# Performance work log

Measured on AMD Instinct MI355X. Metric: run time of the kernel, lower is better.

Reference implementation:

```python
import jax, jax.numpy as jnp
import numpy as np

B, D, F, E, G = 2048, 1024, 4096, 16, 2
EPS = 1e-9
LN_EPS = 1e-5


def setup_inputs() -> dict:
    key = jax.random.key(0)
    ks = jax.random.split(key, 10)
    s_in = 1.0 / np.sqrt(D)
    s_out = 1.0 / np.sqrt(F)
    return {
        "cycle_curve_data": jax.random.normal(ks[0], (B, D), jnp.float32),
        "logits": jax.random.normal(ks[1], (B, E), jnp.float32),
        "moe_masks": jax.random.randint(ks[2], (B, E), 0, 2, jnp.int32),
        "ew_in": jax.random.uniform(ks[3], (E, D, F), jnp.float32, -s_in, s_in),
        "ew_out": jax.random.uniform(ks[4], (E, F, D), jnp.float32, -s_out, s_out),
        "eb_out": jax.random.uniform(ks[5], (E, D), jnp.float32, -s_out, s_out),
        "gw_in": jax.random.uniform(ks[6], (G, D, F), jnp.float32, -s_in, s_in),
        "gw_out": jax.random.uniform(ks[7], (G, F, D), jnp.float32, -s_out, s_out),
        "gb_out": jax.random.uniform(ks[8], (G, D), jnp.float32, -s_out, s_out),
        "ln_gamma": jnp.ones((D,), jnp.float32),
        "ln_beta": jnp.zeros((D,), jnp.float32),
    }


def _moe_forward(x, logits, moe_masks, ew_in, ew_out, eb_out, gw_in, gw_out, gb_out, ln_gamma, ln_beta):
    b = x.shape[0]
    mask = (moe_masks == 1).astype(logits.dtype)          # [B,E]
    raw = jax.nn.softmax(logits, axis=1)                   # [B,E]
    gates = raw * mask
    gates = gates / (jnp.sum(gates, axis=1, keepdims=True) + EPS)
    # Per-expert MLPBlockGELU over all tokens; gate=0 zeroes out non-dispatched
    # tokens exactly as MOEDispatcher.combine does.
    h = jax.nn.gelu(jnp.einsum('bd,edf->ebf', x, ew_in), approximate=False)  # [E,B,F]
    eout = jnp.einsum('ebf,efd->ebd', h, ew_out) + eb_out[:, None, :]        # [E,B,D]
    moe_out = jnp.einsum('be,ebd->bd', gates, eout).astype(jnp.bfloat16)     # combine + bf16 cast
    # general experts (dense, added to routed output; bf16+f32 promotes to f32)
    gh = jax.nn.gelu(jnp.einsum('bd,gdf->gbf', x, gw_in), approximate=False)
    gout = jnp.einsum('gbf,gfd->gbd', gh, gw_out) + gb_out[:, None, :]       # [G,B,D]
    final = jnp.sum(gout, axis=0) + moe_out                                  # f32
    # residual + LayerNorm
    y = final + x
    mu = jnp.mean(y, axis=-1, keepdims=True)
    var = jnp.mean(jnp.square(y - mu), axis=-1, keepdims=True)
    final_out = (y - mu) * jax.lax.rsqrt(var + LN_EPS) * ln_gamma + ln_beta
    # training losses
    expert_logits = jnp.mean(raw, axis=0)                                    # [E]
    expert_sample_count = jnp.sum((gates != 0).astype(raw.dtype), axis=0) / b
    aug_loss = jnp.mean(expert_logits * expert_sample_count)
    s = jnp.sum(raw * mask) / b
    guide_loss = (1.0 - s) * (1.0 - s)
    return final_out, aug_loss, guide_loss


def reference(cycle_curve_data, logits, moe_masks, ew_in, ew_out, eb_out, gw_in, gw_out, gb_out, ln_gamma, ln_beta):
    return _moe_forward(cycle_curve_data, logits, moe_masks, ew_in, ew_out, eb_out,
                        gw_in, gw_out, gb_out, ln_gamma, ln_beta)
```

## Files before the change

kernel.cpp:

```cpp
#include <hip/hip_runtime.h>
#include <hip/hip_bf16.h>

#define B_TOK 2048
#define DDIM 1024
#define FDIM 4096
#define NE 16
#define NG 2
#define BD ((long)B_TOK * DDIM)

typedef unsigned short u16;
typedef __attribute__((ext_vector_type(8))) short bf16x8;
typedef __attribute__((ext_vector_type(4))) float f32x4;

__device__ inline u16 f2bf(float x) {
  union { float f; unsigned u; } v; v.f = x;
  return (u16)((v.u + 0x7fffu + ((v.u >> 16) & 1u)) >> 16);
}
__device__ inline float bfround(float x) {
  union { float f; unsigned u; } v; v.f = x;
  v.u = ((v.u + 0x7fffu + ((v.u >> 16) & 1u)) >> 16) << 16;
  return v.f;
}
__device__ inline float fast_erf(float x) {
  float ax = fabsf(x);
  float t = __builtin_amdgcn_rcpf(1.0f + 0.3275911f * ax);
  float poly = t * (0.254829592f + t * (-0.284496736f + t * (1.421413741f +
               t * (-1.453152027f + t * 1.061405429f))));
  float r = 1.0f - poly * __expf(-ax * ax);
  return copysignf(r, x);
}
__device__ inline float gelu_exact(float x) {
  return 0.5f * x * (1.0f + fast_erf(x * 0.70710678118654752440f));
}
__device__ inline void gload16(const void* g, void* l) {
  __builtin_amdgcn_global_load_lds((const __attribute__((address_space(1))) void*)g,
                                   (__attribute__((address_space(3))) void*)l, 16, 0, 0);
}
__device__ inline float waveSum(float v) {
  v += __shfl_down(v, 32); v += __shfl_down(v, 16); v += __shfl_down(v, 8);
  v += __shfl_down(v, 4);  v += __shfl_down(v, 2);  v += __shfl_down(v, 1);
  return v;
}

__global__ __launch_bounds__(256) void gating_kernel(
    const float* __restrict__ logits, const int* __restrict__ masks,
    float* __restrict__ gates, float* __restrict__ loss)
{
  const int b = blockIdx.x * 256 + threadIdx.x;
  const int lane = threadIdx.x & 63;
  const float* lr = logits + (long)b * NE;
  const int*   mr = masks  + (long)b * NE;
  float raw[NE]; int mk[NE];
  float mx = -1e30f;
#pragma unroll
  for (int e = 0; e < NE; ++e) { raw[e] = lr[e]; mx = fmaxf(mx, raw[e]); }
  float s = 0.f;
#pragma unroll
  for (int e = 0; e < NE; ++e) { raw[e] = expf(raw[e] - mx); s += raw[e]; }
  float inv = 1.0f / s;
#pragma unroll
  for (int e = 0; e < NE; ++e) raw[e] *= inv;
  float gs = 0.f;
#pragma unroll
  for (int e = 0; e < NE; ++e) { mk[e] = (mr[e] == 1); gs += mk[e] ? raw[e] : 0.f; }
  float ginv = 1.0f / (gs + 1e-9f);
  float* gr = gates + (long)b * NE;
#pragma unroll
  for (int e = 0; e < NE; ++e) gr[e] = (mk[e] ? raw[e] : 0.f) * ginv;
#pragma unroll
  for (int e = 0; e < NE; ++e) {
    float cs = waveSum(raw[e]);
    float cc = waveSum(mk[e] ? 1.f : 0.f);
    if (lane == 0) { atomicAdd(&loss[e], cs); atomicAdd(&loss[NE + e], cc); }
  }
  float t = waveSum(gs);
  if (lane == 0) atomicAdd(&loss[32], t);
}

__global__ void finalize_loss(const float* __restrict__ loss, float* __restrict__ out2) {
  if (threadIdx.x == 0) {
    float aug = 0.f;
    for (int e = 0; e < NE; ++e)
      aug += (loss[e] / (float)B_TOK) * (loss[NE + e] / (float)B_TOK);
    aug *= (1.0f / NE);
    float s = loss[32] / (float)B_TOK;
    out2[0] = aug;
    out2[1] = (1.f - s) * (1.f - s);
  }
}

__global__ __launch_bounds__(256) void compact_kernel(
    const int* __restrict__ masks, int* __restrict__ tok,
    int* __restrict__ pos, int* __restrict__ cnts)
{
  const int e = blockIdx.x, tid = threadIdx.x;
  const int lane = tid & 63, wave = tid >> 6;
  __shared__ int wcnt[4];
  __shared__ int runbase;
  if (tid == 0) runbase = 0;
  __syncthreads();
  for (int b0 = 0; b0 < B_TOK; b0 += 256) {
    int b = b0 + tid;
    int m = (masks[(long)b * NE + e] == 1);
    unsigned long long bal = __ballot(m);
    int pre = __popcll(bal & ((1ull << lane) - 1ull));
    if (lane == 0) wcnt[wave] = __popcll(bal);
    __syncthreads();
    int base = runbase;
    for (int w = 0; w < wave; ++w) base += wcnt[w];
    if (m) {
      int p = base + pre;
      tok[(e << 11) + p] = b;
      pos[(long)b * NE + e] = p;
    } else {
      pos[(long)b * NE + e] = -1;
    }
    __syncthreads();
    if (tid == 0) runbase += wcnt[0] + wcnt[1] + wcnt[2] + wcnt[3];
    __syncthreads();
  }
  const int cnt = runbase;
  const int cnt_pad = (cnt + 255) & ~255;
  for (int i = cnt + tid; i < cnt_pad; i += 256)
    tok[(e << 11) + i] = 0;
  if (tid == 0) { cnts[e] = cnt; cnts[NE + e] = cnt_pad; }
}

__global__ __launch_bounds__(256) void cvt_x_kernel(const float* __restrict__ x, u16* __restrict__ xb) {
  long i = ((long)blockIdx.x * 256 + threadIdx.x) * 4;
  float4 v = *(const float4*)&x[i];
  ushort4 o; o.x = f2bf(v.x); o.y = f2bf(v.y); o.z = f2bf(v.z); o.w = f2bf(v.w);
  *(ushort4*)&xb[i] = o;
}

__global__ __launch_bounds__(256) void bias_init_kernel(
    const float* __restrict__ gates, const float* __restrict__ eb,
    float* __restrict__ moe_bias)
{
  long i = (long)blockIdx.x * 256 + threadIdx.x;
  int b = (int)(i >> 10), d = (int)(i & 1023);
  const float* gr = gates + (long)b * NE;
  float s = 0.f;
#pragma unroll
  for (int e = 0; e < NE; ++e) s += gr[e] * eb[e * DDIM + d];
  moe_bias[i] = s;
}

__global__ __launch_bounds__(256) void transpose_cvt(
    const float* __restrict__ src, u16* __restrict__ dst,
    int R, int C, long sZ, long dZ)
{
  __shared__ float t[64][65];
  const float* s = src + (long)blockIdx.z * sZ;
  u16* d = dst + (long)blockIdx.z * dZ;
  const int c0 = blockIdx.x * 64, r0 = blockIdx.y * 64;
  const int tid = threadIdx.x;
#pragma unroll
  for (int it = 0; it < 4; ++it) {
    int idx = tid + it * 256;
    int r = idx >> 4, cq = (idx & 15) * 4;
    float4 v = *(const float4*)&s[(long)(r0 + r) * C + c0 + cq];
    t[r][cq] = v.x; t[r][cq + 1] = v.y; t[r][cq + 2] = v.z; t[r][cq + 3] = v.w;
  }
  __syncthreads();
#pragma unroll
  for (int it = 0; it < 4; ++it) {
    int idx = tid + it * 256;
    int c = idx >> 4, rq = (idx & 15) * 4;
    ushort4 o;
    o.x = f2bf(t[rq][c]); o.y = f2bf(t[rq+1][c]); o.z = f2bf(t[rq+2][c]); o.w = f2bf(t[rq+3][c]);
    *(ushort4*)&d[(long)(c0 + c) * R + r0 + rq] = o;
  }
}

template<int PROJ>
__global__ __launch_bounds__(512, 2) void gemm256(
    const u16* __restrict__ A, int lda, long aZ,
    const u16* __restrict__ Bm, int ldb,
    int klen,
    u16* __restrict__ H,
    float* __restrict__ Eout, float* __restrict__ genp,
    const int* __restrict__ tok, const int* __restrict__ cnts)
{
  constexpr int BN    = PROJ ? 128 : 256;
  constexpr int NBS   = BN / 64;
  constexpr int DEPTH = PROJ ? 2 : 1;
  constexpr int NBUF  = DEPTH + 1;
  constexpr int WN    = BN / 64;
  constexpr int MI    = PROJ ? 4 : 8;
  __shared__ u16 lds[NBUF][16384 + BN * 64];

  int lin = ((int)blockIdx.z * gridDim.x + blockIdx.x) * gridDim.y + blockIdx.y;
  const int T = gridDim.x * gridDim.y * gridDim.z;
  lin = (lin & 7) * (T >> 3) + (lin >> 3);
  const int by = lin % gridDim.y;  int tmp = lin / gridDim.y;
  const int bx = tmp % gridDim.x;  const int z = tmp / gridDim.x;

  const int m0 = by * 256, n0 = bx * BN;
  if (z < NE && m0 >= cnts[NE + z]) return;

  const int tid = threadIdx.x, lane = tid & 63, wave = tid >> 6;
  const int wr = wave / WN, wc = wave % WN;
  const int srow = wave * 8 + (lane >> 3);
  const int swz  = ((lane & 7) * 8) ^ ((lane >> 3) * 8);

  const u16* aSrc[4];
  const u16* bSrc[NBS];
  const u16* Bz = Bm + (long)z * ((long)DDIM * FDIM);
#pragma unroll
  for (int s = 0; s < 4; ++s) {
    int r = m0 + s * 64 + srow;
    if (PROJ == 0 && z < NE) r = tok[(z << 11) + r];
    const u16* Abase = (PROJ == 0) ? A : A + (long)z * aZ;
    aSrc[s] = Abase + (long)r * lda + swz;
  }
#pragma unroll
  for (int s = 0; s < NBS; ++s)
    bSrc[s] = Bz + (long)(n0 + s * 64 + srow) * ldb + swz;

  auto STAGE = [&](int buf, int kk) {
    u16* la = &lds[buf][0];
    u16* lb = &lds[buf][16384];
#pragma unroll
    for (int s = 0; s < 4; ++s)
      gload16(aSrc[s] + kk, la + s * 4096 + wave * 512);
#pragma unroll
    for (int s = 0; s < NBS; ++s)
      gload16(bSrc[s] + kk, lb + s * 4096 + wave * 512);
  };

  f32x4 zero = {0.f, 0.f, 0.f, 0.f};
  f32x4 acc[MI][4];
#pragma unroll
  for (int mi = 0; mi < MI; ++mi)
#pragma unroll
    for (int ni = 0; ni < 4; ++ni) acc[mi][ni] = zero;

  auto COMPUTE = [&](int buf) {
    const u16* la = &lds[buf][0];
    const u16* lb = &lds[buf][16384];
#pragma unroll
    for (int k2 = 0; k2 < 2; ++k2) {
      const int fk = (lane >> 4) * 8 + k2 * 32;
      bf16x8 bv[4];
#pragma unroll
      for (int ni = 0; ni < 4; ++ni) {
        int br = wc * 64 + ni * 16 + (lane & 15);
        bv[ni] = *(const bf16x8*)(lb + br * 64 + (fk ^ ((br & 7) << 3)));
      }
#pragma unroll
      for (int mi = 0; mi < MI; ++mi) {
        int ar = wr * (MI * 16) + mi * 16 + (lane & 15);
        bf16x8 av = *(const bf16x8*)(la + ar * 64 + (fk ^ ((ar & 7) << 3)));
#pragma unroll
        for (int ni = 0; ni < 4; ++ni)
          acc[mi][ni] = __builtin_amdgcn_mfma_f32_16x16x32_bf16(av, bv[ni], acc[mi][ni], 0, 0, 0);
      }
    }
  };

  const int NT = klen >> 6;
  STAGE(0, 0);
  if (DEPTH == 2) STAGE(1, 64);
  int cur = 0, stg = DEPTH;
  for (int t = 0; t < NT; ++t) {
    const int ahead = t + DEPTH;
    if (ahead < NT) {
      STAGE(stg, ahead << 6);
      if (PROJ) asm volatile("s_waitcnt vmcnt(12)" ::: "memory");
      else      asm volatile("s_waitcnt vmcnt(8)"  ::: "memory");
    } else if (PROJ == 1 && t + 1 < NT) {
      asm volatile("s_waitcnt vmcnt(6)" ::: "memory");
    } else {
      asm volatile("s_waitcnt vmcnt(0)" ::: "memory");
    }
    __builtin_amdgcn_s_barrier();
    asm volatile("" ::: "memory");
    COMPUTE(cur);
    asm volatile("" ::: "memory");
    __builtin_amdgcn_s_barrier();
    asm volatile("" ::: "memory");
    cur = (cur + 1 == NBUF) ? 0 : cur + 1;
    stg = (stg + 1 == NBUF) ? 0 : stg + 1;
  }

  const int er = m0 + wr * (MI * 16) + (lane >> 4) * 4;
  const int ec = n0 + wc * 64 + (lane & 15);
  if (PROJ == 0) {
    u16* Hz = H + (long)z * ((long)B_TOK * FDIM);
#pragma unroll
    for (int mi = 0; mi < MI; ++mi)
#pragma unroll
      for (int ni = 0; ni < 4; ++ni) {
        f32x4 v = acc[mi][ni];
        int rb = er + mi * 16, cb = ec + ni * 16;
#pragma unroll
        for (int j = 0; j < 4; ++j)
          Hz[(long)(rb + j) * FDIM + cb] = f2bf(gelu_exact(v[j]));
      }
  } else {
    float* Cz = (z < NE) ? (Eout + (long)z * BD) : (genp + (long)(z - NE) * BD);
#pragma unroll
    for (int mi = 0; mi < MI; ++mi)
#pragma unroll
      for (int ni = 0; ni < 4; ++ni) {
        f32x4 v = acc[mi][ni];
        int rb = er + mi * 16, cb = ec + ni * 16;
#pragma unroll
        for (int j = 0; j < 4; ++j)
          Cz[(long)(rb + j) * DDIM + cb] = v[j];
      }
  }
}

__global__ __launch_bounds__(256) void combine_ln_kernel(
    const float* __restrict__ x, const float* __restrict__ moe_bias,
    const float* __restrict__ Eout, const float* __restrict__ gen_p,
    const float* __restrict__ gb,
    const int* __restrict__ pos, const float* __restrict__ gates,
    const float* __restrict__ gamma, const float* __restrict__ beta,
    float* __restrict__ out)
{
  const int b = blockIdx.x, tid = threadIdx.x;
  const int lane = tid & 63, wave = tid >> 6;
  const long base = (long)b * DDIM;
  __shared__ int posr[NE];
  __shared__ float gr[NE];
  __shared__ float red[4];
  if (tid < NE) { posr[tid] = pos[(long)b * NE + tid]; gr[tid] = gates[(long)b * NE + tid]; }
  __syncthreads();
  float y[4];
  float ls = 0.f;
#pragma unroll
  for (int i = 0; i < 4; ++i) {
    int d = tid + i * 256;
    long idx = base + d;
    float moe = moe_bias[idx];
#pragma unroll
    for (int e = 0; e < NE; ++e) {
      int p = posr[e];
      if (p >= 0) moe += gr[e] * Eout[((long)e * B_TOK + p) * DDIM + d];
    }
    moe = bfround(moe);
    float ge = gb[d] + gb[DDIM + d] + gen_p[idx] + gen_p[BD + idx];
    y[i] = moe + ge + x[idx];
    ls += y[i];
  }
  float t = waveSum(ls);
  if (lane == 0) red[wave] = t;
  __syncthreads();
  float mean = (red[0] + red[1] + red[2] + red[3]) * (1.0f / DDIM);
  __syncthreads();
  float vs = 0.f;
#pragma unroll
  for (int i = 0; i < 4; ++i) { float d2 = y[i] - mean; vs += d2 * d2; }
  t = waveSum(vs);
  if (lane == 0) red[wave] = t;
  __syncthreads();
  float var = (red[0] + red[1] + red[2] + red[3]) * (1.0f / DDIM);
  float inv = rsqrtf(var + 1e-5f);
#pragma unroll
  for (int i = 0; i < 4; ++i) {
    int d = tid + i * 256;
    out[base + d] = (y[i] - mean) * inv * gamma[d] + beta[d];
  }
}

extern "C" void kernel_launch(void* const* d_in, const int* in_sizes, int n_in,
                              void* d_out, int out_size, void* d_ws, size_t ws_size,
                              hipStream_t stream)
{
  const float* x      = (const float*)d_in[0];
  const float* logits = (const float*)d_in[1];
  const int*   masks  = (const int*)d_in[2];
  const float* ew_in  = (const float*)d_in[3];
  const float* ew_out = (const float*)d_in[4];
  const float* eb_out = (const float*)d_in[5];
  const float* gw_in  = (const float*)d_in[6];
  const float* gw_out = (const float*)d_in[7];
  const float* gb_out = (const float*)d_in[8];
  const float* gamma  = (const float*)d_in[9];
  const float* beta   = (const float*)d_in[10];
  float* out = (float*)d_out;

  char* w = (char*)d_ws;
  size_t off = 0;
  auto alloc = [&](size_t bytes) -> void* {
    off = (off + 4095) & ~(size_t)4095;
    void* p = w + off; off += bytes; return p;
  };
  const long DF = (long)DDIM * FDIM;
  const long BF = (long)B_TOK * FDIM;
  const int  NZ = NE + NG;

  float* gates    = (float*)alloc((size_t)B_TOK * NE * 4);
  float* loss     = (float*)alloc(64 * 4);
  int*   tok      = (int*)alloc((size_t)NE * B_TOK * 4);
  int*   pos      = (int*)alloc((size_t)B_TOK * NE * 4);
  int*   cnts     = (int*)alloc(2 * NE * 4);
  u16*   xb       = (u16*)alloc((size_t)BD * 2);
  float* moe_bias = (float*)alloc((size_t)BD * 4);
  float* gen_p    = (float*)alloc((size_t)NG * BD * 4);
  float* Eout     = (float*)alloc((size_t)NE * BD * 4);
  u16*   WinT     = (u16*)alloc((size_t)NZ * DF * 2);
  u16*   WoutT    = (u16*)alloc((size_t)NZ * DF * 2);
  u16*   Hb       = (u16*)alloc((size_t)NZ * BF * 2);

  hipMemsetAsync(loss, 0, 64 * 4, stream);
  gating_kernel<<<8, 256, 0, stream>>>(logits, masks, gates, loss);
  finalize_loss<<<1, 64, 0, stream>>>(loss, out + BD);
  compact_kernel<<<NE, 256, 0, stream>>>(masks, tok, pos, cnts);
  cvt_x_kernel<<<2048, 256, 0, stream>>>(x, xb);
  bias_init_kernel<<<8192, 256, 0, stream>>>(gates, eb_out, moe_bias);

  transpose_cvt<<<dim3(FDIM/64, DDIM/64, NE), 256, 0, stream>>>(
      ew_in, WinT, DDIM, FDIM, DF, DF);
  transpose_cvt<<<dim3(FDIM/64, DDIM/64, NG), 256, 0, stream>>>(
      gw_in, WinT + (long)NE * DF, DDIM, FDIM, DF, DF);
  transpose_cvt<<<dim3(DDIM/64, FDIM/64, NE), 256, 0, stream>>>(
      ew_out, WoutT, FDIM, DDIM, DF, DF);
  transpose_cvt<<<dim3(DDIM/64, FDIM/64, NG), 256, 0, stream>>>(
      gw_out, WoutT + (long)NE * DF, FDIM, DDIM, DF, DF);

  gemm256<0><<<dim3(FDIM/256, B_TOK/256, NZ), 512, 0, stream>>>(
      xb, DDIM, 0L, WinT, DDIM, DDIM,
      Hb, nullptr, nullptr, tok, cnts);
  gemm256<1><<<dim3(DDIM/128, B_TOK/256, NZ), 512, 0, stream>>>(
      Hb, FDIM, BF, WoutT, FDIM, FDIM,
      nullptr, Eout, gen_p, nullptr, cnts);

  combine_ln_kernel<<<B_TOK, 256, 0, stream>>>(
      x, moe_bias, Eout, gen_p, gb_out, pos, gates, gamma, beta, out);
}
```

Measured before the change: 923.6 us.

## Unify GEMM kernels on 256x128 tiles with 3-buffer single-barrier pipeline

Both the up-projection and down-projection GEMMs now use one 256x128 tile configuration with a triple-buffered LDS ring. The per-iteration second barrier is dropped: each iteration waits, syncs once, issues the prefetch for tile t+2, then computes. The fragment loads are restructured so all A/B fragments for both k-halves are read from LDS before the MFMA chain. The up-projection loses its 256-wide tile, which doubles its grid and halves reuse per block, in exchange for deeper prefetch.

```diff
diff --git a/kernel.cpp b/kernel.cpp
--- a/kernel.cpp
+++ b/kernel.cpp
@@ -174,7 +174,7 @@
 }
 
 template<int PROJ>
-__global__ __launch_bounds__(512, 2) void gemm256(
+__global__ __launch_bounds__(512, 2) void gemm256k(
     const u16* __restrict__ A, int lda, long aZ,
     const u16* __restrict__ Bm, int ldb,
     int klen,
@@ -182,13 +182,7 @@
     float* __restrict__ Eout, float* __restrict__ genp,
     const int* __restrict__ tok, const int* __restrict__ cnts)
 {
-  constexpr int BN    = PROJ ? 128 : 256;
-  constexpr int NBS   = BN / 64;
-  constexpr int DEPTH = PROJ ? 2 : 1;
-  constexpr int NBUF  = DEPTH + 1;
-  constexpr int WN    = BN / 64;
-  constexpr int MI    = PROJ ? 4 : 8;
-  __shared__ u16 lds[NBUF][16384 + BN * 64];
+  __shared__ u16 lds[3][24576];
 
   int lin = ((int)blockIdx.z * gridDim.x + blockIdx.x) * gridDim.y + blockIdx.y;
   const int T = gridDim.x * gridDim.y * gridDim.z;
@@ -196,100 +190,96 @@
   const int by = lin % gridDim.y;  int tmp = lin / gridDim.y;
   const int bx = tmp % gridDim.x;  const int z = tmp / gridDim.x;
 
-  const int m0 = by * 256, n0 = bx * BN;
+  const int m0 = by * 256, n0 = bx * 128;
   if (z < NE && m0 >= cnts[NE + z]) return;
 
   const int tid = threadIdx.x, lane = tid & 63, wave = tid >> 6;
-  const int wr = wave / WN, wc = wave % WN;
-  const int srow = wave * 8 + (lane >> 3);
-  const int swz  = ((lane & 7) * 8) ^ ((lane >> 3) * 8);
-
+  const int wr = wave >> 1, wc = wave & 1;
+  const int ln15 = lane & 15, fkb = (lane >> 4) * 8;
+
+  const int swz = ((lane & 7) * 8) ^ ((lane >> 3) * 8);
   const u16* aSrc[4];
-  const u16* bSrc[NBS];
+  const u16* bSrc[2];
   const u16* Bz = Bm + (long)z * ((long)DDIM * FDIM);
 #pragma unroll
   for (int s = 0; s < 4; ++s) {
-    int r = m0 + s * 64 + srow;
+    int r = m0 + s * 64 + wave * 8 + (lane >> 3);
     if (PROJ == 0 && z < NE) r = tok[(z << 11) + r];
     const u16* Abase = (PROJ == 0) ? A : A + (long)z * aZ;
     aSrc[s] = Abase + (long)r * lda + swz;
   }
 #pragma unroll
-  for (int s = 0; s < NBS; ++s)
-    bSrc[s] = Bz + (long)(n0 + s * 64 + srow) * ldb + swz;
-
-  auto STAGE = [&](int buf, int kk) {
-    u16* la = &lds[buf][0];
-    u16* lb = &lds[buf][16384];
-#pragma unroll
-    for (int s = 0; s < 4; ++s)
-      gload16(aSrc[s] + kk, la + s * 4096 + wave * 512);
-#pragma unroll
-    for (int s = 0; s < NBS; ++s)
-      gload16(bSrc[s] + kk, lb + s * 4096 + wave * 512);
+  for (int s = 0; s < 2; ++s)
+    bSrc[s] = Bz + (long)(n0 + s * 64 + wave * 8 + (lane >> 3)) * ldb + swz;
+
+  auto STAGE = [&](int b, int t) {
+    const int kk = t << 6;
+    u16* la = &lds[b][0];
+    u16* lb = &lds[b][16384];
+#pragma unroll
+    for (int s = 0; s < 4; ++s) gload16(aSrc[s] + kk, la + s * 4096 + wave * 512);
+#pragma unroll
+    for (int s = 0; s < 2; ++s) gload16(bSrc[s] + kk, lb + s * 4096 + wave * 512);
   };
 
   f32x4 zero = {0.f, 0.f, 0.f, 0.f};
-  f32x4 acc[MI][4];
-#pragma unroll
-  for (int mi = 0; mi < MI; ++mi)
+  f32x4 acc[4][4];
+#pragma unroll
+  for (int mi = 0; mi < 4; ++mi)
 #pragma unroll
     for (int ni = 0; ni < 4; ++ni) acc[mi][ni] = zero;
 
-  auto COMPUTE = [&](int buf) {
-    const u16* la = &lds[buf][0];
-    const u16* lb = &lds[buf][16384];
-#pragma unroll
-    for (int k2 = 0; k2 < 2; ++k2) {
-      const int fk = (lane >> 4) * 8 + k2 * 32;
-      bf16x8 bv[4];
-#pragma unroll
-      for (int ni = 0; ni < 4; ++ni) {
-        int br = wc * 64 + ni * 16 + (lane & 15);
-        bv[ni] = *(const bf16x8*)(lb + br * 64 + (fk ^ ((br & 7) << 3)));
+  auto COMPUTE = [&](int b) {
+    const u16* la = &lds[b][0];
+    const u16* lb = &lds[b][16384];
+    bf16x8 av[4][2], bv[4][2];
+#pragma unroll
+    for (int mi = 0; mi < 4; ++mi)
+#pragma unroll
+      for (int k2 = 0; k2 < 2; ++k2) {
+        int ar = wr * 64 + mi * 16 + ln15;
+        int fk = fkb + k2 * 32;
+        av[mi][k2] = *(const bf16x8*)(la + ar * 64 + (fk ^ ((ar & 7) << 3)));
       }
 #pragma unroll
-      for (int mi = 0; mi < MI; ++mi) {
-        int ar = wr * (MI * 16) + mi * 16 + (lane & 15);
-        bf16x8 av = *(const bf16x8*)(la + ar * 64 + (fk ^ ((ar & 7) << 3)));
+    for (int ni = 0; ni < 4; ++ni)
+#pragma unroll
+      for (int k2 = 0; k2 < 2; ++k2) {
+        int br = wc * 64 + ni * 16 + ln15;
+        int fk = fkb + k2 * 32;
+        bv[ni][k2] = *(const bf16x8*)(lb + br * 64 + (fk ^ ((br & 7) << 3)));
+      }
+#pragma unroll
+    for (int k2 = 0; k2 < 2; ++k2)
+#pragma unroll
+      for (int mi = 0; mi < 4; ++mi)
 #pragma unroll
         for (int ni = 0; ni < 4; ++ni)
-          acc[mi][ni] = __builtin_amdgcn_mfma_f32_16x16x32_bf16(av, bv[ni], acc[mi][ni], 0, 0, 0);
-      }
-    }
+          acc[mi][ni] = __builtin_amdgcn_mfma_f32_16x16x32_bf16(
+              av[mi][k2], bv[ni][k2], acc[mi][ni], 0, 0, 0);
   };
 
   const int NT = klen >> 6;
   STAGE(0, 0);
-  if (DEPTH == 2) STAGE(1, 64);
-  int cur = 0, stg = DEPTH;
+  STAGE(1, 1);
+  int buf = 0;
   for (int t = 0; t < NT; ++t) {
-    const int ahead = t + DEPTH;
-    if (ahead < NT) {
-      STAGE(stg, ahead << 6);
-      if (PROJ) asm volatile("s_waitcnt vmcnt(12)" ::: "memory");
-      else      asm volatile("s_waitcnt vmcnt(8)"  ::: "memory");
-    } else if (PROJ == 1 && t + 1 < NT) {
-      asm volatile("s_waitcnt vmcnt(6)" ::: "memory");
-    } else {
-      asm volatile("s_waitcnt vmcnt(0)" ::: "memory");
-    }
+    if (t + 1 < NT) asm volatile("s_waitcnt vmcnt(6)" ::: "memory");
+    else            asm volatile("s_waitcnt vmcnt(0)" ::: "memory");
     __builtin_amdgcn_s_barrier();
     asm volatile("" ::: "memory");
-    COMPUTE(cur);
-    asm volatile("" ::: "memory");
-    __builtin_amdgcn_s_barrier();
-    asm volatile("" ::: "memory");
-    cur = (cur + 1 == NBUF) ? 0 : cur + 1;
-    stg = (stg + 1 == NBUF) ? 0 : stg + 1;
-  }
-
-  const int er = m0 + wr * (MI * 16) + (lane >> 4) * 4;
-  const int ec = n0 + wc * 64 + (lane & 15);
+    if (t + 2 < NT) STAGE((t + 2) % 3, t + 2);
+    COMPUTE(buf);
+    asm volatile("s_waitcnt lgkmcnt(0)" ::: "memory");
+    buf = (buf + 1 == 3) ? 0 : buf + 1;
+  }
+
+  const int er = m0 + wr * 64 + (lane >> 4) * 4;
+  const int ec = n0 + wc * 64 + ln15;
   if (PROJ == 0) {
     u16* Hz = H + (long)z * ((long)B_TOK * FDIM);
 #pragma unroll
-    for (int mi = 0; mi < MI; ++mi)
+    for (int mi = 0; mi < 4; ++mi)
 #pragma unroll
       for (int ni = 0; ni < 4; ++ni) {
         f32x4 v = acc[mi][ni];
@@ -301,7 +291,7 @@
   } else {
     float* Cz = (z < NE) ? (Eout + (long)z * BD) : (genp + (long)(z - NE) * BD);
 #pragma unroll
-    for (int mi = 0; mi < MI; ++mi)
+    for (int mi = 0; mi < 4; ++mi)
 #pragma unroll
       for (int ni = 0; ni < 4; ++ni) {
         f32x4 v = acc[mi][ni];
@@ -422,10 +412,10 @@
   transpose_cvt<<<dim3(DDIM/64, FDIM/64, NG), 256, 0, stream>>>(
       gw_out, WoutT + (long)NE * DF, FDIM, DDIM, DF, DF);
 
-  gemm256<0><<<dim3(FDIM/256, B_TOK/256, NZ), 512, 0, stream>>>(
+  gemm256k<0><<<dim3(FDIM/128, B_TOK/256, NZ), 512, 0, stream>>>(
       xb, DDIM, 0L, WinT, DDIM, DDIM,
       Hb, nullptr, nullptr, tok, cnts);
-  gemm256<1><<<dim3(DDIM/128, B_TOK/256, NZ), 512, 0, stream>>>(
+  gemm256k<1><<<dim3(DDIM/128, B_TOK/256, NZ), 512, 0, stream>>>(
       Hb, FDIM, BF, WoutT, FDIM, FDIM,
       nullptr, Eout, gen_p, nullptr, cnts);
 
```

After: 943.1 us. 2.1% more time.
